# Kernel optimization log

Hardware: AMD Instinct MI355X
Metric: run time of the kernel (lower is better)

## Reference

```python
import jax, jax.numpy as jnp
import numpy as np

K = 24          # num_eigh
D_MODEL = 768   # d_in == d_out
STATE = 100     # LDS state_dim
BSZ = 1
SEQ = 2048


def setup_inputs() -> dict:
    key = jax.random.key(0)
    ks = jax.random.split(key, 8)
    x = jax.random.normal(ks[0], (BSZ, SEQ, D_MODEL), dtype=jnp.float32)
    input_pos = jnp.arange(SEQ, dtype=jnp.int32)
    M_inputs = jax.random.normal(ks[1], (D_MODEL, D_MODEL), dtype=jnp.float32) * 0.02
    M_filters = jax.random.normal(ks[2], (K, D_MODEL), dtype=jnp.float32) * 0.02
    # LDS params: diagonal A (stable, |a|<1), B maps scalar input -> state,
    # C maps state -> 2K outputs, Dv is scalar-input feedthrough to 2K outputs.
    A = jax.random.uniform(ks[3], (STATE,), dtype=jnp.float32, minval=0.0, maxval=0.99)
    Bm = jax.random.normal(ks[4], (STATE,), dtype=jnp.float32) * 0.1
    C = jax.random.normal(ks[5], (STATE, 2 * K), dtype=jnp.float32) * 0.1
    Dv = jax.random.normal(ks[6], (2 * K,), dtype=jnp.float32) * 0.1
    return {"x": x, "input_pos": input_pos, "M_inputs": M_inputs,
            "M_filters": M_filters, "A": A, "Bm": Bm, "C": C, "Dv": Dv}


def reference(x, input_pos, M_inputs, M_filters, A, Bm, C, Dv):
    bsz, seq_len, d_in = x.shape
    k = M_filters.shape[0]
    # input projection (use_approx branch)
    xp = x @ M_inputs                                   # (b, s, d)
    # flatten per-channel scalar sequences: (b*d, s)
    u = xp.transpose(0, 2, 1).reshape(bsz * d_in, seq_len)
    ut = u.T                                            # (s, N) for scan over time
    h0 = jnp.zeros((bsz * d_in, A.shape[0]), dtype=xp.dtype)

    def step(h, u_t):
        # h: (N, state), u_t: (N,) scalar input per lane
        h = h * A[None, :] + u_t[:, None] * Bm[None, :]
        y = h @ C + u_t[:, None] * Dv[None, :]          # (N, 2K)
        return h, y

    _, ys = jax.lax.scan(step, h0, ut)                  # (s, N, 2K)
    # U: (b, s, 2K, d)
    U = ys.transpose(1, 0, 2).reshape(bsz, d_in, seq_len, 2 * k).transpose(0, 2, 3, 1)
    spectral_plus = jnp.einsum('bskd,kd->bsd', U[:, :, k:, :], M_filters)
    spectral_minus = jnp.einsum('bskd,kd->bsd', U[:, :, :k, :], M_filters)
    return spectral_plus + spectral_minus
```

## Files before the change

kernel.cpp:

```cpp
#include <hip/hip_runtime.h>

#define SEQ   2048
#define DM    768
#define ST    100
#define KF    24
#define NC    32
#define KJ    128
#define NJ    112

using half8   = __attribute__((ext_vector_type(8))) _Float16;
using float4v = __attribute__((ext_vector_type(4))) float;
using ush8    = __attribute__((ext_vector_type(8))) short;

__device__ __forceinline__ unsigned short f2h(float v) {
    union { _Float16 h; unsigned short u; } cv;
    cv.h = (_Float16)v;
    return cv.u;
}
__device__ __forceinline__ void async16(const void* g, void* l) {
    __builtin_amdgcn_global_load_lds(
        (const __attribute__((address_space(1))) unsigned int*)g,
        (__attribute__((address_space(3))) unsigned int*)l, 16, 0, 0);
}

__global__ __launch_bounds__(256) void prep(const float* __restrict__ x,
                                            const float* __restrict__ Mi,
                                            const float* __restrict__ C,
                                            const float* __restrict__ Dv,
                                            const float* __restrict__ Mf,
                                            const float* __restrict__ Av,
                                            const float* __restrict__ Bv,
                                            unsigned short* __restrict__ Mh,
                                            unsigned short* __restrict__ Xh,
                                            float* __restrict__ WpT,
                                            float* __restrict__ evec,
                                            float* __restrict__ Apow,
                                            unsigned short* __restrict__ Eh,
                                            unsigned short* __restrict__ Qh) {
    __shared__ float tl[64][65];
    int bid = blockIdx.x, t = threadIdx.x;
    if (bid < 144) {
        int i0 = (bid / 12) * 64, d0 = (bid % 12) * 64;
        int tx = t & 63, ty = t >> 6;
#pragma unroll
        for (int r = ty; r < 64; r += 4)
            tl[r][tx] = Mi[(i0 + r) * DM + d0 + tx];
        __syncthreads();
#pragma unroll
        for (int r = ty; r < 64; r += 4)
            Mh[(size_t)(d0 + r) * DM + i0 + tx] = f2h(tl[tx][r]);
    } else if (bid < 912) {
        int idx8 = (bid - 144) * 256 + t;
        int s = idx8 / (DM / 8), i0 = (idx8 % (DM / 8)) * 8;
        const float* xp = x + (size_t)s * DM + i0;
        float4 v0 = *(const float4*)xp;
        float4 v1 = *(const float4*)(xp + 4);
        float av[8] = {v0.x, v0.y, v0.z, v0.w, v1.x, v1.y, v1.z, v1.w};
        ush8 hh;
#pragma unroll
        for (int q = 0; q < 8; ++q) hh[q] = (short)f2h(av[q]);
        *(ush8*)(Xh + (size_t)s * DM + i0) = hh;
    } else if (bid < 1212) {
        int tid = (bid - 912) * 256 + t;
        if (tid < ST * DM) {
            int d = tid / ST, j = tid % ST;
            float s = 0.f;
#pragma unroll
            for (int k = 0; k < KF; ++k)
                s += (C[j * 2 * KF + k] + C[j * 2 * KF + KF + k]) * Mf[k * DM + d];
            WpT[tid] = s;
        }
        if (tid < DM) {
            float s = 0.f;
#pragma unroll
            for (int k = 0; k < KF; ++k)
                s += (Dv[k] + Dv[KF + k]) * Mf[k * DM + tid];
            evec[tid] = s;
        }
    } else {
        if (t < KJ) {
            bool ja = (t < ST);
            float a = ja ? Av[t] : 0.f;
            float b = ja ? Bv[t] : 0.f;
            float p = 1.f;
            for (int dlt = 0; dlt < 64; ++dlt) {
                if (ja) Apow[dlt * ST + t] = p;
                if (t < NJ) Qh[t * 64 + 63 - dlt] = f2h(b * p);
                p *= a;
                Eh[dlt * KJ + t] = f2h(p);
            }
            if (ja) Apow[64 * ST + t] = p;
        }
    }
}

__global__ __launch_bounds__(256) void gemm_mfma(const unsigned short* __restrict__ Mh,
                                                 const unsigned short* __restrict__ Xh,
                                                 float* __restrict__ ut) {
    __shared__ unsigned short As[2][64 * 64];
    __shared__ unsigned short Bs[2][64 * 64];
    int t = threadIdx.x;
    int tile = blockIdx.x;
    int d0 = (tile % (DM / 64)) * 64;
    int s0 = (tile / (DM / 64)) * 64;
    int wave = t >> 6, lane = t & 63;
    int m16 = lane & 15, quad = lane >> 4;
    int r0 = t >> 3,         q0 = ((t & 7) - r0) & 7;
    int r1 = (t + 256) >> 3, q1 = (((t + 256) & 7) - r1) & 7;
    float4v acc[4];
#pragma unroll
    for (int nt = 0; nt < 4; ++nt) acc[nt] = (float4v){0.f, 0.f, 0.f, 0.f};

#define STAGE(buf, kk0)                                                                     \
    async16(&Mh[(size_t)(d0 + r0) * DM + (kk0) + q0 * 8], &As[buf][(size_t)t * 8]);         \
    async16(&Xh[(size_t)(s0 + r0) * DM + (kk0) + q0 * 8], &Bs[buf][(size_t)t * 8]);         \
    async16(&Mh[(size_t)(d0 + r1) * DM + (kk0) + q1 * 8], &As[buf][(size_t)(t + 256) * 8]); \
    async16(&Xh[(size_t)(s0 + r1) * DM + (kk0) + q1 * 8], &Bs[buf][(size_t)(t + 256) * 8]);

    STAGE(0, 0);
    __syncthreads();
    int cur = 0;
    int arow = wave * 16 + m16;
    for (int k0 = 0; k0 < DM; k0 += 64) {
        if (k0 + 64 < DM) { STAGE(cur ^ 1, k0 + 64); }
        half8 af[2], bf[4][2];
#pragma unroll
        for (int h = 0; h < 2; ++h)
            af[h] = *(half8*)&As[cur][arow * 64 + (((h * 4 + quad) + arow) & 7) * 8];
#pragma unroll
        for (int nt = 0; nt < 4; ++nt) {
            int brow = nt * 16 + m16;
#pragma unroll
            for (int h = 0; h < 2; ++h)
                bf[nt][h] = *(half8*)&Bs[cur][brow * 64 + (((h * 4 + quad) + brow) & 7) * 8];
        }
#pragma unroll
        for (int h = 0; h < 2; ++h)
#pragma unroll
            for (int nt = 0; nt < 4; ++nt)
                acc[nt] = __builtin_amdgcn_mfma_f32_16x16x32_f16(af[h], bf[nt][h], acc[nt], 0, 0, 0);
        __syncthreads();
        cur ^= 1;
    }
#undef STAGE
#pragma unroll
    for (int nt = 0; nt < 4; ++nt) {
        int dd = d0 + wave * 16 + quad * 4;
        int ss = s0 + nt * 16 + m16;
#pragma unroll
        for (int i = 0; i < 4; ++i)
            ut[(size_t)(dd + i) * SEQ + ss] = acc[nt][i];
    }
}

__global__ __launch_bounds__(256) void scanf_k(float* ut,
                                               const unsigned short* __restrict__ Qh,
                                               const float* __restrict__ WpT,
                                               const float* __restrict__ Apow,
                                               const float* __restrict__ Bv,
                                               const float* __restrict__ evec,
                                               unsigned short* __restrict__ Gh) {
    __shared__ float hl[64][120];
    __shared__ float kk[128];
    __shared__ float ul[2][32][65];
    int t = threadIdx.x;
    int m0 = blockIdx.x * 64;
    int d0 = blockIdx.x * 2;
    if (t < 128) {
        int dlt = t & 63, dloc = t >> 6;
        const float* wrow = WpT + (d0 + dloc) * ST;
        float s = 0.f;
        for (int j = 0; j < ST; ++j)
            s = fmaf(Bv[j] * Apow[dlt * ST + j], wrow[j], s);
        kk[t] = s;
    }
    int wave = t >> 6, lane = t & 63;
    int m16 = lane & 15, quad = lane >> 4;
    {
        int r = wave * 16 + m16;
        float4v acc[7];
#pragma unroll
        for (int nt = 0; nt < 7; ++nt) acc[nt] = (float4v){0.f, 0.f, 0.f, 0.f};
#pragma unroll
        for (int ks = 0; ks < 2; ++ks) {
            size_t ao = (size_t)(m0 + r) * 64 + ks * 32 + quad * 8;
            float4 a0 = *(const float4*)(ut + ao);
            float4 a1 = *(const float4*)(ut + ao + 4);
            *(float4*)&ul[r >> 5][r & 31][ks * 32 + quad * 8]     = a0;
            *(float4*)&ul[r >> 5][r & 31][ks * 32 + quad * 8 + 4] = a1;
            float av[8] = {a0.x, a0.y, a0.z, a0.w, a1.x, a1.y, a1.z, a1.w};
            half8 ah;
#pragma unroll
            for (int q = 0; q < 8; ++q) ah[q] = (_Float16)av[q];
#pragma unroll
            for (int nt = 0; nt < 7; ++nt) {
                half8 bh = *(const half8*)(Qh + (nt * 16 + m16) * 64 + ks * 32 + quad * 8);
                acc[nt] = __builtin_amdgcn_mfma_f32_16x16x32_f16(ah, bh, acc[nt], 0, 0, 0);
            }
        }
#pragma unroll
        for (int nt = 0; nt < 7; ++nt)
#pragma unroll
            for (int i = 0; i < 4; ++i)
                hl[wave * 16 + quad * 4 + i][nt * 16 + m16] = acc[nt][i];
    }
    __syncthreads();
    {
        int j = t & 127, dloc = t >> 7;
        int d = d0 + dloc;
        bool ja = (j < ST);
        float a64 = ja ? Apow[64 * ST + j] : 0.f;
        float w   = ja ? WpT[d * ST + j] : 0.f;
        float hs = 0.f;
        for (int c = 0; c < NC; ++c) {
            Gh[((size_t)c * DM + d) * KJ + j] = f2h(w * hs);
            float add = ja ? hl[dloc * 32 + c][j] : 0.f;
            hs = fmaf(a64, hs, add);
        }
    }
    {
        int q = wave;
        int p = t & 63;
        int dloc = p >> 5, c = p & 31;
        int d = d0 + dloc;
        int lo0 = q * 8, hi0 = (7 - q) * 8;
        const float* kt = &kk[dloc * 64];
        const float* us = &ul[dloc][c][0];
        float e = evec[d];
        float ylo[8], yhi[8];
#pragma unroll
        for (int z = 0; z < 8; ++z) {
            ylo[z] = e * us[lo0 + z];
            yhi[z] = e * us[hi0 + z];
        }
        for (int i = 0; i < lo0; ++i) {
            float u = us[i];
#pragma unroll
            for (int z = 0; z < 8; ++z) {
                ylo[z] = fmaf(kt[lo0 + z - i], u, ylo[z]);
                yhi[z] = fmaf(kt[hi0 + z - i], u, yhi[z]);
            }
        }
#pragma unroll
        for (int zi = 0; zi < 8; ++zi) {
            float u = us[lo0 + zi];
#pragma unroll
            for (int z = zi; z < 8; ++z)
                ylo[z] = fmaf(kt[z - zi], u, ylo[z]);
#pragma unroll
            for (int z = 0; z < 8; ++z)
                yhi[z] = fmaf(kt[hi0 - lo0 + z - zi], u, yhi[z]);
        }
        for (int i = lo0 + 8; i < hi0; ++i) {
            float u = us[i];
#pragma unroll
            for (int z = 0; z < 8; ++z)
                yhi[z] = fmaf(kt[hi0 + z - i], u, yhi[z]);
        }
#pragma unroll
        for (int zi = 0; zi < 8; ++zi) {
            float u = us[hi0 + zi];
#pragma unroll
            for (int z = zi; z < 8; ++z)
                yhi[z] = fmaf(kt[z - zi], u, yhi[z]);
        }
        size_t off = (size_t)d * SEQ + c * 64;
        *(float4*)(ut + off + lo0)     = make_float4(ylo[0], ylo[1], ylo[2], ylo[3]);
        *(float4*)(ut + off + lo0 + 4) = make_float4(ylo[4], ylo[5], ylo[6], ylo[7]);
        *(float4*)(ut + off + hi0)     = make_float4(yhi[0], yhi[1], yhi[2], yhi[3]);
        *(float4*)(ut + off + hi0 + 4) = make_float4(yhi[4], yhi[5], yhi[6], yhi[7]);
    }
}

__global__ __launch_bounds__(256) void inter(const unsigned short* __restrict__ Eh,
                                             const unsigned short* __restrict__ Gh,
                                             const float* __restrict__ yintra,
                                             float* __restrict__ out) {
    __shared__ float yl[64][65];
    int c = blockIdx.x;
    int d0 = blockIdx.y * 64;
    int t = threadIdx.x;
#pragma unroll
    for (int it = 0; it < 4; ++it) {
        int idx = t + it * 256;
        int row = idx >> 4, col4 = (idx & 15) * 4;
        float4 v = *(const float4*)&yintra[(size_t)(d0 + row) * SEQ + c * 64 + col4];
        yl[col4 + 0][row] = v.x;
        yl[col4 + 1][row] = v.y;
        yl[col4 + 2][row] = v.z;
        yl[col4 + 3][row] = v.w;
    }
    __syncthreads();
    int wave = t >> 6, lane = t & 63;
    int wn = wave * 16;
    int m16 = lane & 15, quad = lane >> 4;
    float4v acc[4];
#pragma unroll
    for (int mt = 0; mt < 4; ++mt) acc[mt] = (float4v){0.f, 0.f, 0.f, 0.f};
#pragma unroll
    for (int ks = 0; ks < 4; ++ks) {
        half8 bh = *(const half8*)(Gh + ((size_t)c * DM + d0 + wn + m16) * KJ + ks * 32 + quad * 8);
#pragma unroll
        for (int mt = 0; mt < 4; ++mt) {
            half8 ah = *(const half8*)(Eh + (mt * 16 + m16) * KJ + ks * 32 + quad * 8);
            acc[mt] = __builtin_amdgcn_mfma_f32_16x16x32_f16(ah, bh, acc[mt], 0, 0, 0);
        }
    }
#pragma unroll
    for (int mt = 0; mt < 4; ++mt) {
        int tt = mt * 16 + quad * 4;
        int dcol = wn + m16;
#pragma unroll
        for (int i = 0; i < 4; ++i) {
            float v = acc[mt][i] + yl[tt + i][dcol];
            out[(size_t)(c * 64 + tt + i) * DM + d0 + dcol] = v;
        }
    }
}

extern "C" void kernel_launch(void* const* d_in, const int* in_sizes, int n_in,
                              void* d_out, int out_size, void* d_ws, size_t ws_size,
                              hipStream_t stream) {
    const float* x  = (const float*)d_in[0];
    const float* Mi = (const float*)d_in[2];
    const float* Mf = (const float*)d_in[3];
    const float* Av = (const float*)d_in[4];
    const float* Bv = (const float*)d_in[5];
    const float* C  = (const float*)d_in[6];
    const float* Dv = (const float*)d_in[7];
    float* out = (float*)d_out;

    float* ut   = (float*)d_ws;
    float* WpT  = ut + (size_t)DM * SEQ;
    float* ev   = WpT + DM * ST;
    float* Apow = ev + DM;
    unsigned short* Mh = (unsigned short*)(Apow + 65 * ST);
    unsigned short* Xh = Mh + (size_t)DM * DM;
    unsigned short* Eh = Xh + (size_t)SEQ * DM;
    unsigned short* Qh = Eh + 64 * KJ;
    unsigned short* Gh = Qh + NJ * 64;

    prep<<<1213, 256, 0, stream>>>(x, Mi, C, Dv, Mf, Av, Bv, Mh, Xh,
                                   WpT, ev, Apow, Eh, Qh);
    gemm_mfma<<<(DM / 64) * (SEQ / 64), 256, 0, stream>>>(Mh, Xh, ut);
    scanf_k<<<384, 256, 0, stream>>>(ut, Qh, WpT, Apow, Bv, ev, Gh);
    inter<<<dim3(NC, DM / 64), 256, 0, stream>>>(Eh, Gh, ut, out);
}
```

Before: 117.7 us.

## Triple-buffer GEMM async loads and precompute scan kernel taps in prep

The projection GEMM moves from a double-buffered loop with two barriers per step to a three-stage async global-to-LDS pipeline. It uses explicit vmcnt/lgkmcnt waits and a single barrier per iteration, which lets loads run further ahead of the MFMAs. Separately, the per-channel 64-tap kernel (sum over state of W·B·A^dlt) moves out of the scan kernel's prologue into 192 extra prep blocks that write it to a workspace buffer Kt. The scan kernel then just loads those taps. The cost is more LDS per GEMM block and more prep blocks.

```diff
diff --git a/kernel.cpp b/kernel.cpp
--- a/kernel.cpp
+++ b/kernel.cpp
@@ -36,8 +36,11 @@
                                             float* __restrict__ evec,
                                             float* __restrict__ Apow,
                                             unsigned short* __restrict__ Eh,
-                                            unsigned short* __restrict__ Qh) {
+                                            unsigned short* __restrict__ Qh,
+                                            float* __restrict__ Kt) {
     __shared__ float tl[64][65];
+    __shared__ float Wl[4][100];
+    __shared__ float ApB[100][65];
     int bid = blockIdx.x, t = threadIdx.x;
     if (bid < 144) {
         int i0 = (bid / 12) * 64, d0 = (bid % 12) * 64;
@@ -77,7 +80,7 @@
                 s += (Dv[k] + Dv[KF + k]) * Mf[k * DM + tid];
             evec[tid] = s;
         }
-    } else {
+    } else if (bid == 1212) {
         if (t < KJ) {
             bool ja = (t < ST);
             float a = ja ? Av[t] : 0.f;
@@ -91,14 +94,34 @@
             }
             if (ja) Apow[64 * ST + t] = p;
         }
+    } else {
+        int d0k = (bid - 1213) * 4;
+        for (int idx = t; idx < 4 * ST; idx += 256) {
+            int dl = idx / ST, j = idx % ST;
+            float s = 0.f;
+#pragma unroll
+            for (int k = 0; k < KF; ++k)
+                s += (C[j * 2 * KF + k] + C[j * 2 * KF + KF + k]) * Mf[k * DM + d0k + dl];
+            Wl[dl][j] = s;
+        }
+        if (t < ST) {
+            float a = Av[t], p = Bv[t];
+            for (int dlt = 0; dlt < 64; ++dlt) { ApB[t][dlt] = p; p *= a; }
+        }
+        __syncthreads();
+        int dl = t >> 6, dlt = t & 63;
+        float s = 0.f;
+        for (int j = 0; j < ST; ++j)
+            s = fmaf(Wl[dl][j], ApB[j][dlt], s);
+        Kt[(d0k + dl) * 64 + dlt] = s;
     }
 }
 
 __global__ __launch_bounds__(256) void gemm_mfma(const unsigned short* __restrict__ Mh,
                                                  const unsigned short* __restrict__ Xh,
                                                  float* __restrict__ ut) {
-    __shared__ unsigned short As[2][64 * 64];
-    __shared__ unsigned short Bs[2][64 * 64];
+    __shared__ unsigned short As[3][64 * 64];
+    __shared__ unsigned short Bs[3][64 * 64];
     int t = threadIdx.x;
     int tile = blockIdx.x;
     int d0 = (tile % (DM / 64)) * 64;
@@ -118,11 +141,17 @@
     async16(&Xh[(size_t)(s0 + r1) * DM + (kk0) + q1 * 8], &Bs[buf][(size_t)(t + 256) * 8]);
 
     STAGE(0, 0);
-    __syncthreads();
-    int cur = 0;
+    STAGE(1, 64);
     int arow = wave * 16 + m16;
-    for (int k0 = 0; k0 < DM; k0 += 64) {
-        if (k0 + 64 < DM) { STAGE(cur ^ 1, k0 + 64); }
+#pragma unroll
+    for (int it = 0; it < 12; ++it) {
+        const int cur = it % 3;
+        const int sb  = (it + 2) % 3;
+        asm volatile("s_waitcnt lgkmcnt(0)" ::: "memory");
+        if (it < 10) asm volatile("s_waitcnt vmcnt(4)" ::: "memory");
+        else         asm volatile("s_waitcnt vmcnt(0)" ::: "memory");
+        __builtin_amdgcn_s_barrier();
+        if (it < 10) { STAGE(sb, it * 64 + 128); }
         half8 af[2], bf[4][2];
 #pragma unroll
         for (int h = 0; h < 2; ++h)
@@ -139,8 +168,6 @@
 #pragma unroll
             for (int nt = 0; nt < 4; ++nt)
                 acc[nt] = __builtin_amdgcn_mfma_f32_16x16x32_f16(af[h], bf[nt][h], acc[nt], 0, 0, 0);
-        __syncthreads();
-        cur ^= 1;
     }
 #undef STAGE
 #pragma unroll
@@ -157,23 +184,17 @@
                                                const unsigned short* __restrict__ Qh,
                                                const float* __restrict__ WpT,
                                                const float* __restrict__ Apow,
-                                               const float* __restrict__ Bv,
                                                const float* __restrict__ evec,
-                                               unsigned short* __restrict__ Gh) {
+                                               unsigned short* __restrict__ Gh,
+                                               const float* __restrict__ Kt) {
     __shared__ float hl[64][120];
     __shared__ float kk[128];
     __shared__ float ul[2][32][65];
     int t = threadIdx.x;
     int m0 = blockIdx.x * 64;
     int d0 = blockIdx.x * 2;
-    if (t < 128) {
-        int dlt = t & 63, dloc = t >> 6;
-        const float* wrow = WpT + (d0 + dloc) * ST;
-        float s = 0.f;
-        for (int j = 0; j < ST; ++j)
-            s = fmaf(Bv[j] * Apow[dlt * ST + j], wrow[j], s);
-        kk[t] = s;
-    }
+    if (t < 128)
+        kk[t] = Kt[(d0 + (t >> 6)) * 64 + (t & 63)];
     int wave = t >> 6, lane = t & 63;
     int m16 = lane & 15, quad = lane >> 4;
     {
@@ -339,10 +360,11 @@
     unsigned short* Eh = Xh + (size_t)SEQ * DM;
     unsigned short* Qh = Eh + 64 * KJ;
     unsigned short* Gh = Qh + NJ * 64;
-
-    prep<<<1213, 256, 0, stream>>>(x, Mi, C, Dv, Mf, Av, Bv, Mh, Xh,
-                                   WpT, ev, Apow, Eh, Qh);
+    float* Kt = (float*)(Gh + (size_t)NC * DM * KJ);
+
+    prep<<<1405, 256, 0, stream>>>(x, Mi, C, Dv, Mf, Av, Bv, Mh, Xh,
+                                   WpT, ev, Apow, Eh, Qh, Kt);
     gemm_mfma<<<(DM / 64) * (SEQ / 64), 256, 0, stream>>>(Mh, Xh, ut);
-    scanf_k<<<384, 256, 0, stream>>>(ut, Qh, WpT, Apow, Bv, ev, Gh);
+    scanf_k<<<384, 256, 0, stream>>>(ut, Qh, WpT, Apow, ev, Gh, Kt);
     inter<<<dim3(NC, DM / 64), 256, 0, stream>>>(Eh, Gh, ut, out);
 }
```

Measured after the change: 115.3 us. 1.02x faster.
